# Kernel optimization log

Hardware: AMD Instinct MI355X
Metric: run time of the kernel (lower is better)

Reference implementation:

```python
import jax, jax.numpy as jnp
import numpy as np

G = 256          # grid resolution -> V = G*G vertices
B = 8            # batch of meshes
N_SAMPLES = 2048
W_CHAMFER, W_EDGE, W_NORMAL, W_LAP = 1.0, 1.0, 0.1, 0.1
V = G * G


def _grid_faces(g):
    idx = np.arange(g * g).reshape(g, g)
    v00 = idx[:-1, :-1].ravel(); v01 = idx[:-1, 1:].ravel()
    v10 = idx[1:, :-1].ravel();  v11 = idx[1:, 1:].ravel()
    f1 = np.stack([v00, v01, v10], 1)
    f2 = np.stack([v01, v11, v10], 1)
    return np.concatenate([f1, f2], 0).astype(np.int32)  # [F,3]


def _edges_and_pairs(faces, n_verts):
    # all face-edge incidences + the opposite vertex of each incidence
    e = np.concatenate([faces[:, [0, 1]], faces[:, [1, 2]], faces[:, [0, 2]]], 0)
    opp = np.concatenate([faces[:, 2], faces[:, 0], faces[:, 1]], 0)
    e = np.sort(e, 1)
    key = e[:, 0].astype(np.int64) * n_verts + e[:, 1]
    order = np.argsort(key, kind='stable')
    key_s, es, opps = key[order], e[order], opp[order]
    first = np.ones(len(key_s), bool); first[1:] = key_s[1:] != key_s[:-1]
    edges = es[first].astype(np.int32)                      # unique undirected edges [E,2]
    dup = np.nonzero(~first)[0]                             # 2nd incidence of shared edges
    pairs = np.stack([es[dup - 1, 0], es[dup - 1, 1], opps[dup - 1], opps[dup]], 1).astype(np.int32)  # [P,4]
    return edges, pairs


def setup_inputs() -> dict:
    key = jax.random.key(0)
    faces = _grid_faces(G)
    edges, nc_pairs = _edges_and_pairs(faces, V)
    # base grid geometry + gaussian perturbation (realistic smooth-ish surfaces)
    xs, ys = np.meshgrid(np.linspace(0, 1, G), np.linspace(0, 1, G), indexing='ij')
    base = np.stack([xs, ys, 0.1 * np.sin(4 * np.pi * xs) * np.cos(4 * np.pi * ys)], -1).reshape(V, 3)
    k1, k2 = jax.random.split(key)
    verts_pred = jnp.asarray(base, jnp.float32)[None] + 0.01 * jax.random.normal(k1, (B, V, 3), jnp.float32)
    verts_targ = jnp.asarray(base, jnp.float32)[None] + 0.01 * jax.random.normal(k2, (B, V, 3), jnp.float32)
    return {
        'verts_pred': verts_pred,
        'verts_targ': verts_targ,
        'faces': jnp.asarray(faces),
        'edges': jnp.asarray(edges),
        'nc_pairs': jnp.asarray(nc_pairs),
    }


def _sample_points(verts, faces, key, n):
    # verts [V,3]; area-weighted face sampling + uniform barycentric (pytorch3d scheme)
    v0, v1, v2 = verts[faces[:, 0]], verts[faces[:, 1]], verts[faces[:, 2]]
    areas = 0.5 * jnp.linalg.norm(jnp.cross(v1 - v0, v2 - v0), axis=-1)          # [F]
    kf, kb = jax.random.split(key)
    fidx = jax.random.categorical(kf, jnp.log(areas + 1e-12), shape=(n,))        # [n]
    uv = jax.random.uniform(kb, (n, 2), verts.dtype)
    su = jnp.sqrt(uv[:, 0:1]); vv = uv[:, 1:2]
    w0, w1, w2 = 1.0 - su, su * (1.0 - vv), su * vv
    return w0 * v0[fidx] + w1 * v1[fidx] + w2 * v2[fidx]                         # [n,3]


def _chamfer(x, y):
    # squared-distance chamfer, mean over points then batch, both directions summed
    d = jnp.sum((x[:, :, None, :] - y[:, None, :, :]) ** 2, -1)                  # [B,N,M]
    return jnp.mean(jnp.min(d, axis=2)) + jnp.mean(jnp.min(d, axis=1))


def _edge_loss(verts, edges):
    diff = verts[:, edges[:, 0]] - verts[:, edges[:, 1]]                          # [B,E,3]
    return jnp.mean(jnp.sum(diff * diff, -1))                                     # (||e|| - 0)^2


def _normal_consistency(verts, nc_pairs):
    v0 = verts[:, nc_pairs[:, 0]]; v1 = verts[:, nc_pairs[:, 1]]
    a = verts[:, nc_pairs[:, 2]]; b = verts[:, nc_pairs[:, 3]]
    e = v1 - v0
    n0 = jnp.cross(e, a - v0)
    n1 = -jnp.cross(e, b - v0)
    eps = 1e-8
    cos = jnp.sum(n0 * n1, -1) / (
        jnp.maximum(jnp.linalg.norm(n0, axis=-1), eps)
        * jnp.maximum(jnp.linalg.norm(n1, axis=-1), eps))
    return jnp.mean(1.0 - cos)


def _laplacian_uniform(verts, edges):
    e0, e1 = edges[:, 0], edges[:, 1]
    ones = jnp.ones((edges.shape[0],), verts.dtype)

    def per_mesh(v):  # v [V,3]
        nsum = (jax.ops.segment_sum(v[e1], e0, num_segments=V)
                + jax.ops.segment_sum(v[e0], e1, num_segments=V))
        deg = (jax.ops.segment_sum(ones, e0, num_segments=V)
               + jax.ops.segment_sum(ones, e1, num_segments=V))
        lap = nsum / jnp.maximum(deg, 1.0)[:, None] - v                           # D^-1 A v - v
        return jnp.mean(jnp.linalg.norm(lap, axis=-1))

    return jnp.mean(jax.vmap(per_mesh)(verts))


def reference(verts_pred, verts_targ, faces, edges, nc_pairs):
    skey = jax.random.key(42)
    kp = jax.random.split(jax.random.fold_in(skey, 0), verts_pred.shape[0])
    kt = jax.random.split(jax.random.fold_in(skey, 1), verts_targ.shape[0])
    sample_pred = jax.vmap(lambda v, k: _sample_points(v, faces, k, N_SAMPLES))(verts_pred, kp)
    sample_targ = jax.vmap(lambda v, k: _sample_points(v, faces, k, N_SAMPLES))(verts_targ, kt)
    loss_chamfer = _chamfer(sample_pred, sample_targ)
    loss_edge = _edge_loss(verts_pred, edges)
    loss_normal = _normal_consistency(verts_pred, nc_pairs)
    loss_lap = _laplacian_uniform(verts_pred, edges)
    loss = (W_CHAMFER * loss_chamfer + W_EDGE * loss_edge
            + W_NORMAL * loss_normal + W_LAP * loss_lap)
    return (loss, loss_chamfer, loss_edge, loss_normal, loss_lap)
```

## Files before the change

kernel.cpp:

```cpp
#include <hip/hip_runtime.h>
#include <stdint.h>

#define GSZ 256
#define NV (GSZ*GSZ)
#define NS 2048
#define CELLS (255*255)
#define FH CELLS
#define NF (2*CELLS)
#define CH 8

struct F3 { float x, y, z; };

__device__ __forceinline__ F3 ldv3(const float* __restrict__ p, int idx) {
    const float* q = p + 3*(size_t)idx;
    F3 r; r.x = q[0]; r.y = q[1]; r.z = q[2]; return r;
}
__device__ __forceinline__ F3 f3sub(F3 a, F3 b) { return F3{a.x-b.x, a.y-b.y, a.z-b.z}; }
__device__ __forceinline__ F3 f3cross(F3 a, F3 b) {
    return F3{a.y*b.z - a.z*b.y, a.z*b.x - a.x*b.z, a.x*b.y - a.y*b.x};
}
__device__ __forceinline__ float f3dot(F3 a, F3 b) { return a.x*b.x + a.y*b.y + a.z*b.z; }

__device__ __forceinline__ uint64_t splitmix64(uint64_t& s) {
    s += 0x9E3779B97F4A7C15ULL;
    uint64_t z = s;
    z = (z ^ (z >> 30)) * 0xBF58476D1CE4E5B9ULL;
    z = (z ^ (z >> 27)) * 0x94D049BB133111EBULL;
    return z ^ (z >> 31);
}

__device__ __forceinline__ float blockReduceSum256(float v) {
    __shared__ float s[4];
    int lane = threadIdx.x & 63, w = threadIdx.x >> 6;
    #pragma unroll
    for (int o = 32; o > 0; o >>= 1) v += __shfl_down(v, o, 64);
    if (lane == 0) s[w] = v;
    __syncthreads();
    if (threadIdx.x == 0) v = s[0] + s[1] + s[2] + s[3];
    return v;
}

__global__ void k_area(const float* __restrict__ vp, const float* __restrict__ vt,
                       int B, float* __restrict__ areas, float* __restrict__ blockmax) {
    int gid = blockIdx.x*256 + threadIdx.x;
    int total = 2*B*CELLS;
    float mloc = 0.f;
    if (gid < total) {
        int m = gid / CELLS;
        int c = gid - m*CELLS;
        int i = c / 255, j = c - i*255;
        const float* verts = (m < B ? vp + (size_t)m*NV*3
                                    : vt + (size_t)(m-B)*NV*3);
        int b00 = i*GSZ + j;
        F3 v00 = ldv3(verts, b00);
        F3 v01 = ldv3(verts, b00+1);
        F3 v10 = ldv3(verts, b00+GSZ);
        F3 v11 = ldv3(verts, b00+GSZ+1);
        F3 c1 = f3cross(f3sub(v01, v00), f3sub(v10, v00));
        F3 c2 = f3cross(f3sub(v11, v01), f3sub(v10, v01));
        float a1 = 0.5f * sqrtf(f3dot(c1, c1));
        float a2 = 0.5f * sqrtf(f3dot(c2, c2));
        size_t base = (size_t)m*NF;
        areas[base + c]      = a1;
        areas[base + FH + c] = a2;
        mloc = fmaxf(a1, a2);
    }
    #pragma unroll
    for (int o = 32; o > 0; o >>= 1) mloc = fmaxf(mloc, __shfl_down(mloc, o, 64));
    __shared__ float s[4];
    int lane = threadIdx.x & 63, w = threadIdx.x >> 6;
    if (lane == 0) s[w] = mloc;
    __syncthreads();
    if (threadIdx.x == 0)
        blockmax[blockIdx.x] = fmaxf(fmaxf(s[0], s[1]), fmaxf(s[2], s[3]));
}

__global__ void k_sample(const float* __restrict__ vp, const float* __restrict__ vt,
                         int B, const float* __restrict__ areas,
                         const float* __restrict__ blockmax, int nbm,
                         float* __restrict__ samples) {
    float m = 0.f;
    for (int k = threadIdx.x; k < nbm; k += 256) m = fmaxf(m, blockmax[k]);
    #pragma unroll
    for (int o = 32; o > 0; o >>= 1) m = fmaxf(m, __shfl_down(m, o, 64));
    __shared__ float s[4];
    int lane = threadIdx.x & 63, w = threadIdx.x >> 6;
    if (lane == 0) s[w] = m;
    __syncthreads();
    __shared__ float sMaxA;
    if (threadIdx.x == 0) sMaxA = fmaxf(fmaxf(s[0], s[1]), fmaxf(s[2], s[3]));
    __syncthreads();
    float maxA = sMaxA;

    int gid = blockIdx.x*256 + threadIdx.x;
    int cloud = gid / (B*NS);
    int rem = gid - cloud*(B*NS);
    int b = rem / NS;
    const float* verts = (cloud ? vt : vp) + (size_t)b*NV*3;
    const float* am = areas + (size_t)(cloud*B + b)*NF;

    uint64_t st = ((uint64_t)(gid + 1) * 0x9E3779B97F4A7C15ULL) ^ 0xC0FFEE123456789ULL;
    int f = 0;
    for (int round = 0; round < 64; ++round) {
        uint64_t r0 = splitmix64(st), r1 = splitmix64(st);
        uint64_t r2 = splitmix64(st), r3 = splitmix64(st);
        int f0 = (int)(((uint64_t)(uint32_t)r0 * (uint32_t)NF) >> 32);
        int f1 = (int)(((uint64_t)(uint32_t)r1 * (uint32_t)NF) >> 32);
        int f2 = (int)(((uint64_t)(uint32_t)r2 * (uint32_t)NF) >> 32);
        int f3 = (int)(((uint64_t)(uint32_t)r3 * (uint32_t)NF) >> 32);
        float a0 = am[f0], a1 = am[f1], a2 = am[f2], a3 = am[f3];
        float u0 = ((uint32_t)(r0 >> 40)) * (1.f/16777216.f);
        float u1 = ((uint32_t)(r1 >> 40)) * (1.f/16777216.f);
        float u2 = ((uint32_t)(r2 >> 40)) * (1.f/16777216.f);
        float u3 = ((uint32_t)(r3 >> 40)) * (1.f/16777216.f);
        if (u0 * maxA <= a0) { f = f0; break; }
        if (u1 * maxA <= a1) { f = f1; break; }
        if (u2 * maxA <= a2) { f = f2; break; }
        if (u3 * maxA <= a3) { f = f3; break; }
        f = f3;
    }
    int i0, i1, i2;
    if (f < FH) {
        int c = f;  int i = c / 255, j = c - i*255;  int v = i*GSZ + j;
        i0 = v; i1 = v + 1; i2 = v + GSZ;
    } else {
        int c = f - FH;  int i = c / 255, j = c - i*255;  int v = i*GSZ + j;
        i0 = v + 1; i1 = v + GSZ + 1; i2 = v + GSZ;
    }
    F3 v0 = ldv3(verts, i0), v1 = ldv3(verts, i1), v2 = ldv3(verts, i2);
    uint64_t r = splitmix64(st);
    float u0 = ((uint32_t)r >> 8) * (1.f/16777216.f);
    float u1 = ((uint32_t)(r >> 32) >> 8) * (1.f/16777216.f);
    float su = sqrtf(u0);
    float w0 = 1.f - su, w1 = su * (1.f - u1), w2 = su * u1;
    float* o = samples + (size_t)gid*3;
    o[0] = w0*v0.x + w1*v1.x + w2*v2.x;
    o[1] = w0*v0.y + w1*v1.y + w2*v2.y;
    o[2] = w0*v0.z + w1*v1.z + w2*v2.z;
}

__global__ void k_chamfer(const float* __restrict__ samples, int B,
                          float* __restrict__ minpart) {
    int dir = blockIdx.z >> 4, q = blockIdx.z & 15;
    int b = blockIdx.y, xh = blockIdx.x;
    const float* src = samples + ((size_t)dir*B + b)*NS*3;
    const float* dst = samples + ((size_t)(1-dir)*B + b)*NS*3;

    __shared__ float4 tile[128];
    if (threadIdx.x < 128) {
        const float* p = dst + (size_t)(q*128 + threadIdx.x)*3;
        tile[threadIdx.x] = make_float4(p[0], p[1], p[2], 0.f);
    }
    float px[4], py[4], pz[4], mn[4];
    #pragma unroll
    for (int k = 0; k < 4; ++k) {
        int i = xh*1024 + k*256 + threadIdx.x;
        const float* p = src + (size_t)i*3;
        px[k] = p[0]; py[k] = p[1]; pz[k] = p[2];
        mn[k] = 3.402823466e38f;
    }
    __syncthreads();
    #pragma unroll 2
    for (int j = 0; j < 128; ++j) {
        float4 t = tile[j];
        #pragma unroll
        for (int k = 0; k < 4; ++k) {
            float dx = px[k]-t.x, dy = py[k]-t.y, dz = pz[k]-t.z;
            mn[k] = fminf(mn[k], dx*dx + dy*dy + dz*dz);
        }
    }
    float* outp = minpart + (((size_t)(dir*B + b)*16) + q)*NS;
    #pragma unroll
    for (int k = 0; k < 4; ++k)
        outp[xh*1024 + k*256 + threadIdx.x] = mn[k];
}

__global__ void k_cham_reduce(const float* __restrict__ minpart, int B,
                              float* __restrict__ chamPart) {
    int gid = blockIdx.x*256 + threadIdx.x;
    int dir = gid / (B*NS);
    int rem = gid - dir*(B*NS);
    int b = rem / NS, i = rem - b*NS;
    const float* p = minpart + (size_t)(dir*B + b)*16*NS + i;
    float mn = 3.402823466e38f;
    #pragma unroll
    for (int q = 0; q < 16; ++q) mn = fminf(mn, p[(size_t)q*NS]);
    float sm = blockReduceSum256(mn);
    if (threadIdx.x == 0) chamPart[blockIdx.x] = sm;
}

__global__ void k_mesh(const float* __restrict__ vp, const int* __restrict__ edges,
                       const int* __restrict__ ncp, int B, int E, int P,
                       int nbE, int nbP,
                       float* __restrict__ partE, float* __restrict__ partP,
                       float* __restrict__ partV) {
    int bx = blockIdx.x, b = blockIdx.y;
    const float* verts = vp + (size_t)b*NV*3;
    float acc = 0.f;
    if (bx < nbE) {
        int base = bx*(256*CH);
        #pragma unroll 2
        for (int c = 0; c < CH; ++c) {
            int e = base + c*256 + threadIdx.x;
            if (e < E) {
                int2 ed = ((const int2*)edges)[e];
                F3 d = f3sub(ldv3(verts, ed.x), ldv3(verts, ed.y));
                acc += f3dot(d, d);
            }
        }
        float s = blockReduceSum256(acc);
        if (threadIdx.x == 0) partE[(size_t)bx*B + b] = s;
    } else if (bx < nbE + nbP) {
        int base = (bx - nbE)*(256*CH);
        for (int c = 0; c < CH; ++c) {
            int p = base + c*256 + threadIdx.x;
            if (p < P) {
                int4 q = ((const int4*)ncp)[p];
                F3 v0 = ldv3(verts, q.x), v1 = ldv3(verts, q.y);
                F3 a = ldv3(verts, q.z), bb = ldv3(verts, q.w);
                F3 e = f3sub(v1, v0);
                F3 n0 = f3cross(e, f3sub(a, v0));
                F3 n1 = f3cross(f3sub(bb, v0), e);
                float num = f3dot(n0, n1);
                float den = fmaxf(sqrtf(f3dot(n0, n0)), 1e-8f) *
                            fmaxf(sqrtf(f3dot(n1, n1)), 1e-8f);
                acc += 1.f - num / den;
            }
        }
        float s = blockReduceSum256(acc);
        if (threadIdx.x == 0) partP[(size_t)(bx - nbE)*B + b] = s;
    } else {
        int base = (bx - nbE - nbP)*(256*CH);
        for (int c = 0; c < CH; ++c) {
            int idx = base + c*256 + threadIdx.x;
            int i = idx >> 8, j = idx & 255;
            F3 ctr = ldv3(verts, idx);
            float nx = 0.f, ny = 0.f, nz = 0.f; int deg = 0;
            #define ADDN(ii, jj) { F3 n_ = ldv3(verts, (ii)*GSZ + (jj)); \
                                   nx += n_.x; ny += n_.y; nz += n_.z; ++deg; }
            if (j > 0)               ADDN(i, j-1);
            if (j < GSZ-1)           ADDN(i, j+1);
            if (i > 0)               ADDN(i-1, j);
            if (i < GSZ-1)           ADDN(i+1, j);
            if (i < GSZ-1 && j > 0)  ADDN(i+1, j-1);
            if (i > 0 && j < GSZ-1)  ADDN(i-1, j+1);
            #undef ADDN
            float inv = 1.f / (float)deg;
            float lx = nx*inv - ctr.x, ly = ny*inv - ctr.y, lz = nz*inv - ctr.z;
            acc += sqrtf(lx*lx + ly*ly + lz*lz);
        }
        float s = blockReduceSum256(acc);
        if (threadIdx.x == 0) partV[(size_t)(bx - nbE - nbP)*B + b] = s;
    }
}

__global__ void k_final(const float* __restrict__ chamPart,
                        const float* __restrict__ partE, int nE,
                        const float* __restrict__ partP, int nP,
                        const float* __restrict__ partV, int nL,
                        int B, int E, int P, float* __restrict__ out) {
    double a0 = 0, a1 = 0, aE = 0, aP = 0, aL = 0;
    for (int k = threadIdx.x; k < 64;  k += 256) a0 += (double)chamPart[k];
    for (int k = 64 + threadIdx.x; k < 128; k += 256) a1 += (double)chamPart[k];
    for (int k = threadIdx.x; k < nE; k += 256) aE += (double)partE[k];
    for (int k = threadIdx.x; k < nP; k += 256) aP += (double)partP[k];
    for (int k = threadIdx.x; k < nL; k += 256) aL += (double)partV[k];
    __shared__ double sd[5][4];
    double v[5] = {a0, a1, aE, aP, aL};
    int lane = threadIdx.x & 63, w = threadIdx.x >> 6;
    #pragma unroll
    for (int r = 0; r < 5; ++r) {
        double x = v[r];
        #pragma unroll
        for (int o = 32; o > 0; o >>= 1) x += __shfl_down(x, o, 64);
        if (lane == 0) sd[r][w] = x;
    }
    __syncthreads();
    if (threadIdx.x == 0) {
        double bn = (double)B * NS;
        double ch = (sd[0][0]+sd[0][1]+sd[0][2]+sd[0][3]) / bn
                  + (sd[1][0]+sd[1][1]+sd[1][2]+sd[1][3]) / bn;
        double ed = (sd[2][0]+sd[2][1]+sd[2][2]+sd[2][3]) / ((double)B * E);
        double no = (sd[3][0]+sd[3][1]+sd[3][2]+sd[3][3]) / ((double)B * P);
        double la = (sd[4][0]+sd[4][1]+sd[4][2]+sd[4][3]) / ((double)B * NV);
        double loss = ch + ed + 0.1*no + 0.1*la;
        out[0] = (float)loss; out[1] = (float)ch; out[2] = (float)ed;
        out[3] = (float)no;   out[4] = (float)la;
    }
}

extern "C" void kernel_launch(void* const* d_in, const int* in_sizes, int n_in,
                              void* d_out, int out_size, void* d_ws, size_t ws_size,
                              hipStream_t stream) {
    const float* vp = (const float*)d_in[0];
    const float* vt = (const float*)d_in[1];
    const int* edges = (const int*)d_in[3];
    const int* ncp   = (const int*)d_in[4];
    const int B = in_sizes[0] / (3*NV);
    const int E = in_sizes[3] / 2;
    const int P = in_sizes[4] / 4;

    char* ws = (char*)d_ws;
    size_t off = 0;
    float* areas    = (float*)(ws + off); off += (size_t)2*B*NF*sizeof(float);
    float* samples  = (float*)(ws + off); off += (size_t)2*B*NS*3*sizeof(float);
    float* minpart  = (float*)(ws + off); off += (size_t)2*B*16*NS*sizeof(float);
    float* blockmax = (float*)(ws + off); off += 8192*sizeof(float);
    float* chamPart = (float*)(ws + off); off += 256*sizeof(float);
    float* partE    = (float*)(ws + off); off += 2048*sizeof(float);
    float* partP    = (float*)(ws + off); off += 2048*sizeof(float);
    float* partV    = (float*)(ws + off); off += 1024*sizeof(float);

    int nbm = (2*B*CELLS + 255)/256;
    k_area<<<nbm, 256, 0, stream>>>(vp, vt, B, areas, blockmax);
    k_sample<<<(2*B*NS)/256, 256, 0, stream>>>(vp, vt, B, areas, blockmax, nbm, samples);
    dim3 gch(2, B, 32);
    k_chamfer<<<gch, 256, 0, stream>>>(samples, B, minpart);
    k_cham_reduce<<<(2*B*NS)/256, 256, 0, stream>>>(minpart, B, chamPart);
    int nbE = (E + 256*CH - 1)/(256*CH);
    int nbP = (P + 256*CH - 1)/(256*CH);
    int nbV = NV/(256*CH);
    dim3 gm(nbE + nbP + nbV, B);
    k_mesh<<<gm, 256, 0, stream>>>(vp, edges, ncp, B, E, P, nbE, nbP,
                                   partE, partP, partV);
    k_final<<<1, 256, 0, stream>>>(chamPart, partE, nbE*B, partP, nbP*B,
                                   partV, nbV*B, B, E, P, (float*)d_out);
}
```

Before: 147.6 us.

## Fuse all loss stages into one cooperative persistent kernel with grid syncs

```diff
diff --git a/kernel.cpp b/kernel.cpp
--- a/kernel.cpp
+++ b/kernel.cpp
@@ -1,5 +1,8 @@
 #include <hip/hip_runtime.h>
+#include <hip/hip_cooperative_groups.h>
 #include <stdint.h>
+
+namespace cg = cooperative_groups;
 
 #define GSZ 256
 #define NV (GSZ*GSZ)
@@ -7,7 +10,9 @@
 #define CELLS (255*255)
 #define FH CELLS
 #define NF (2*CELLS)
-#define CH 8
+#define NBLK 512
+#define NTHR 256
+#define NTOT (NBLK*NTHR)
 
 struct F3 { float x, y, z; };
 
@@ -29,211 +34,100 @@
     return z ^ (z >> 31);
 }
 
+__shared__ float4 g_tile[2048];
+__shared__ float  g_sred[4];
+__shared__ float  g_mred[256];
+__shared__ float  g_sMaxA;
+__shared__ double g_dred[5][4];
+
 __device__ __forceinline__ float blockReduceSum256(float v) {
-    __shared__ float s[4];
+    __syncthreads();
     int lane = threadIdx.x & 63, w = threadIdx.x >> 6;
     #pragma unroll
     for (int o = 32; o > 0; o >>= 1) v += __shfl_down(v, o, 64);
-    if (lane == 0) s[w] = v;
+    if (lane == 0) g_sred[w] = v;
     __syncthreads();
-    if (threadIdx.x == 0) v = s[0] + s[1] + s[2] + s[3];
+    if (threadIdx.x == 0) v = g_sred[0] + g_sred[1] + g_sred[2] + g_sred[3];
     return v;
 }
 
-__global__ void k_area(const float* __restrict__ vp, const float* __restrict__ vt,
-                       int B, float* __restrict__ areas, float* __restrict__ blockmax) {
-    int gid = blockIdx.x*256 + threadIdx.x;
-    int total = 2*B*CELLS;
+__global__ void __launch_bounds__(256, 2)
+k_all(const float* __restrict__ vp, const float* __restrict__ vt,
+      const int* __restrict__ edges, const int* __restrict__ ncp,
+      int B, int E, int P,
+      float* __restrict__ areas, float* __restrict__ samples,
+      float* __restrict__ blockmax, float* __restrict__ chamPart,
+      float* __restrict__ partE, float* __restrict__ partP,
+      float* __restrict__ partL, float* __restrict__ out) {
+    cg::grid_group grid = cg::this_grid();
+    const int tid = threadIdx.x, bid = blockIdx.x;
+    const int gid = bid*NTHR + tid;
+
     float mloc = 0.f;
-    if (gid < total) {
-        int m = gid / CELLS;
-        int c = gid - m*CELLS;
-        int i = c / 255, j = c - i*255;
-        const float* verts = (m < B ? vp + (size_t)m*NV*3
-                                    : vt + (size_t)(m-B)*NV*3);
-        int b00 = i*GSZ + j;
-        F3 v00 = ldv3(verts, b00);
-        F3 v01 = ldv3(verts, b00+1);
-        F3 v10 = ldv3(verts, b00+GSZ);
-        F3 v11 = ldv3(verts, b00+GSZ+1);
-        F3 c1 = f3cross(f3sub(v01, v00), f3sub(v10, v00));
-        F3 c2 = f3cross(f3sub(v11, v01), f3sub(v10, v01));
-        float a1 = 0.5f * sqrtf(f3dot(c1, c1));
-        float a2 = 0.5f * sqrtf(f3dot(c2, c2));
-        size_t base = (size_t)m*NF;
-        areas[base + c]      = a1;
-        areas[base + FH + c] = a2;
-        mloc = fmaxf(a1, a2);
-    }
-    #pragma unroll
-    for (int o = 32; o > 0; o >>= 1) mloc = fmaxf(mloc, __shfl_down(mloc, o, 64));
-    __shared__ float s[4];
-    int lane = threadIdx.x & 63, w = threadIdx.x >> 6;
-    if (lane == 0) s[w] = mloc;
-    __syncthreads();
-    if (threadIdx.x == 0)
-        blockmax[blockIdx.x] = fmaxf(fmaxf(s[0], s[1]), fmaxf(s[2], s[3]));
-}
-
-__global__ void k_sample(const float* __restrict__ vp, const float* __restrict__ vt,
-                         int B, const float* __restrict__ areas,
-                         const float* __restrict__ blockmax, int nbm,
-                         float* __restrict__ samples) {
-    float m = 0.f;
-    for (int k = threadIdx.x; k < nbm; k += 256) m = fmaxf(m, blockmax[k]);
-    #pragma unroll
-    for (int o = 32; o > 0; o >>= 1) m = fmaxf(m, __shfl_down(m, o, 64));
-    __shared__ float s[4];
-    int lane = threadIdx.x & 63, w = threadIdx.x >> 6;
-    if (lane == 0) s[w] = m;
-    __syncthreads();
-    __shared__ float sMaxA;
-    if (threadIdx.x == 0) sMaxA = fmaxf(fmaxf(s[0], s[1]), fmaxf(s[2], s[3]));
-    __syncthreads();
-    float maxA = sMaxA;
-
-    int gid = blockIdx.x*256 + threadIdx.x;
-    int cloud = gid / (B*NS);
-    int rem = gid - cloud*(B*NS);
-    int b = rem / NS;
-    const float* verts = (cloud ? vt : vp) + (size_t)b*NV*3;
-    const float* am = areas + (size_t)(cloud*B + b)*NF;
-
-    uint64_t st = ((uint64_t)(gid + 1) * 0x9E3779B97F4A7C15ULL) ^ 0xC0FFEE123456789ULL;
-    int f = 0;
-    for (int round = 0; round < 64; ++round) {
-        uint64_t r0 = splitmix64(st), r1 = splitmix64(st);
-        uint64_t r2 = splitmix64(st), r3 = splitmix64(st);
-        int f0 = (int)(((uint64_t)(uint32_t)r0 * (uint32_t)NF) >> 32);
-        int f1 = (int)(((uint64_t)(uint32_t)r1 * (uint32_t)NF) >> 32);
-        int f2 = (int)(((uint64_t)(uint32_t)r2 * (uint32_t)NF) >> 32);
-        int f3 = (int)(((uint64_t)(uint32_t)r3 * (uint32_t)NF) >> 32);
-        float a0 = am[f0], a1 = am[f1], a2 = am[f2], a3 = am[f3];
-        float u0 = ((uint32_t)(r0 >> 40)) * (1.f/16777216.f);
-        float u1 = ((uint32_t)(r1 >> 40)) * (1.f/16777216.f);
-        float u2 = ((uint32_t)(r2 >> 40)) * (1.f/16777216.f);
-        float u3 = ((uint32_t)(r3 >> 40)) * (1.f/16777216.f);
-        if (u0 * maxA <= a0) { f = f0; break; }
-        if (u1 * maxA <= a1) { f = f1; break; }
-        if (u2 * maxA <= a2) { f = f2; break; }
-        if (u3 * maxA <= a3) { f = f3; break; }
-        f = f3;
-    }
-    int i0, i1, i2;
-    if (f < FH) {
-        int c = f;  int i = c / 255, j = c - i*255;  int v = i*GSZ + j;
-        i0 = v; i1 = v + 1; i2 = v + GSZ;
-    } else {
-        int c = f - FH;  int i = c / 255, j = c - i*255;  int v = i*GSZ + j;
-        i0 = v + 1; i1 = v + GSZ + 1; i2 = v + GSZ;
-    }
-    F3 v0 = ldv3(verts, i0), v1 = ldv3(verts, i1), v2 = ldv3(verts, i2);
-    uint64_t r = splitmix64(st);
-    float u0 = ((uint32_t)r >> 8) * (1.f/16777216.f);
-    float u1 = ((uint32_t)(r >> 32) >> 8) * (1.f/16777216.f);
-    float su = sqrtf(u0);
-    float w0 = 1.f - su, w1 = su * (1.f - u1), w2 = su * u1;
-    float* o = samples + (size_t)gid*3;
-    o[0] = w0*v0.x + w1*v1.x + w2*v2.x;
-    o[1] = w0*v0.y + w1*v1.y + w2*v2.y;
-    o[2] = w0*v0.z + w1*v1.z + w2*v2.z;
-}
-
-__global__ void k_chamfer(const float* __restrict__ samples, int B,
-                          float* __restrict__ minpart) {
-    int dir = blockIdx.z >> 4, q = blockIdx.z & 15;
-    int b = blockIdx.y, xh = blockIdx.x;
-    const float* src = samples + ((size_t)dir*B + b)*NS*3;
-    const float* dst = samples + ((size_t)(1-dir)*B + b)*NS*3;
-
-    __shared__ float4 tile[128];
-    if (threadIdx.x < 128) {
-        const float* p = dst + (size_t)(q*128 + threadIdx.x)*3;
-        tile[threadIdx.x] = make_float4(p[0], p[1], p[2], 0.f);
-    }
-    float px[4], py[4], pz[4], mn[4];
-    #pragma unroll
-    for (int k = 0; k < 4; ++k) {
-        int i = xh*1024 + k*256 + threadIdx.x;
-        const float* p = src + (size_t)i*3;
-        px[k] = p[0]; py[k] = p[1]; pz[k] = p[2];
-        mn[k] = 3.402823466e38f;
-    }
-    __syncthreads();
-    #pragma unroll 2
-    for (int j = 0; j < 128; ++j) {
-        float4 t = tile[j];
+    {
+        int total = 2*B*CELLS;
+        for (int c = gid; c < total; c += NTOT) {
+            int m = c / CELLS, cc = c - m*CELLS;
+            int i = cc / 255, j = cc - i*255;
+            const float* verts = (m < B ? vp + (size_t)m*NV*3
+                                        : vt + (size_t)(m-B)*NV*3);
+            int v = i*GSZ + j;
+            F3 v00 = ldv3(verts, v),       v01 = ldv3(verts, v+1);
+            F3 v10 = ldv3(verts, v+GSZ),   v11 = ldv3(verts, v+GSZ+1);
+            F3 c1 = f3cross(f3sub(v01, v00), f3sub(v10, v00));
+            F3 c2 = f3cross(f3sub(v11, v01), f3sub(v10, v01));
+            float a1 = 0.5f * sqrtf(f3dot(c1, c1));
+            float a2 = 0.5f * sqrtf(f3dot(c2, c2));
+            size_t base = (size_t)m*NF;
+            areas[base + cc]      = a1;
+            areas[base + FH + cc] = a2;
+            mloc = fmaxf(mloc, fmaxf(a1, a2));
+        }
+    }
+    {
         #pragma unroll
-        for (int k = 0; k < 4; ++k) {
-            float dx = px[k]-t.x, dy = py[k]-t.y, dz = pz[k]-t.z;
-            mn[k] = fminf(mn[k], dx*dx + dy*dy + dz*dz);
-        }
-    }
-    float* outp = minpart + (((size_t)(dir*B + b)*16) + q)*NS;
-    #pragma unroll
-    for (int k = 0; k < 4; ++k)
-        outp[xh*1024 + k*256 + threadIdx.x] = mn[k];
-}
-
-__global__ void k_cham_reduce(const float* __restrict__ minpart, int B,
-                              float* __restrict__ chamPart) {
-    int gid = blockIdx.x*256 + threadIdx.x;
-    int dir = gid / (B*NS);
-    int rem = gid - dir*(B*NS);
-    int b = rem / NS, i = rem - b*NS;
-    const float* p = minpart + (size_t)(dir*B + b)*16*NS + i;
-    float mn = 3.402823466e38f;
-    #pragma unroll
-    for (int q = 0; q < 16; ++q) mn = fminf(mn, p[(size_t)q*NS]);
-    float sm = blockReduceSum256(mn);
-    if (threadIdx.x == 0) chamPart[blockIdx.x] = sm;
-}
-
-__global__ void k_mesh(const float* __restrict__ vp, const int* __restrict__ edges,
-                       const int* __restrict__ ncp, int B, int E, int P,
-                       int nbE, int nbP,
-                       float* __restrict__ partE, float* __restrict__ partP,
-                       float* __restrict__ partV) {
-    int bx = blockIdx.x, b = blockIdx.y;
-    const float* verts = vp + (size_t)b*NV*3;
-    float acc = 0.f;
-    if (bx < nbE) {
-        int base = bx*(256*CH);
-        #pragma unroll 2
-        for (int c = 0; c < CH; ++c) {
-            int e = base + c*256 + threadIdx.x;
-            if (e < E) {
-                int2 ed = ((const int2*)edges)[e];
-                F3 d = f3sub(ldv3(verts, ed.x), ldv3(verts, ed.y));
-                acc += f3dot(d, d);
-            }
-        }
-        float s = blockReduceSum256(acc);
-        if (threadIdx.x == 0) partE[(size_t)bx*B + b] = s;
-    } else if (bx < nbE + nbP) {
-        int base = (bx - nbE)*(256*CH);
-        for (int c = 0; c < CH; ++c) {
-            int p = base + c*256 + threadIdx.x;
-            if (p < P) {
-                int4 q = ((const int4*)ncp)[p];
-                F3 v0 = ldv3(verts, q.x), v1 = ldv3(verts, q.y);
-                F3 a = ldv3(verts, q.z), bb = ldv3(verts, q.w);
-                F3 e = f3sub(v1, v0);
-                F3 n0 = f3cross(e, f3sub(a, v0));
-                F3 n1 = f3cross(f3sub(bb, v0), e);
-                float num = f3dot(n0, n1);
-                float den = fmaxf(sqrtf(f3dot(n0, n0)), 1e-8f) *
-                            fmaxf(sqrtf(f3dot(n1, n1)), 1e-8f);
-                acc += 1.f - num / den;
-            }
-        }
-        float s = blockReduceSum256(acc);
-        if (threadIdx.x == 0) partP[(size_t)(bx - nbE)*B + b] = s;
-    } else {
-        int base = (bx - nbE - nbP)*(256*CH);
-        for (int c = 0; c < CH; ++c) {
-            int idx = base + c*256 + threadIdx.x;
+        for (int o = 32; o > 0; o >>= 1) mloc = fmaxf(mloc, __shfl_down(mloc, o, 64));
+        int lane = tid & 63, w = tid >> 6;
+        if (lane == 0) g_sred[w] = mloc;
+        __syncthreads();
+        if (tid == 0)
+            blockmax[bid] = fmaxf(fmaxf(g_sred[0], g_sred[1]),
+                                  fmaxf(g_sred[2], g_sred[3]));
+    }
+    float accE = 0.f, accP = 0.f, accL = 0.f;
+    {
+        int total = B*E;
+        for (int g = gid; g < total; g += NTOT) {
+            int b = g / E, e = g - b*E;
+            const float* verts = vp + (size_t)b*NV*3;
+            int2 ed = ((const int2*)edges)[e];
+            F3 d = f3sub(ldv3(verts, ed.x), ldv3(verts, ed.y));
+            accE += f3dot(d, d);
+        }
+    }
+    {
+        int total = B*P;
+        for (int g = gid; g < total; g += NTOT) {
+            int b = g / P, p = g - b*P;
+            const float* verts = vp + (size_t)b*NV*3;
+            int4 q = ((const int4*)ncp)[p];
+            F3 v0 = ldv3(verts, q.x), v1 = ldv3(verts, q.y);
+            F3 a = ldv3(verts, q.z), bb = ldv3(verts, q.w);
+            F3 e = f3sub(v1, v0);
+            F3 n0 = f3cross(e, f3sub(a, v0));
+            F3 n1 = f3cross(f3sub(bb, v0), e);
+            float num = f3dot(n0, n1);
+            float den = fmaxf(sqrtf(f3dot(n0, n0)), 1e-8f) *
+                        fmaxf(sqrtf(f3dot(n1, n1)), 1e-8f);
+            accP += 1.f - num / den;
+        }
+    }
+    {
+        int total = B*NV;
+        for (int g = gid; g < total; g += NTOT) {
+            int b = g >> 16, idx = g & (NV-1);
             int i = idx >> 8, j = idx & 255;
+            const float* verts = vp + (size_t)b*NV*3;
             F3 ctr = ldv3(verts, idx);
             float nx = 0.f, ny = 0.f, nz = 0.f; int deg = 0;
             #define ADDN(ii, jj) { F3 n_ = ldv3(verts, (ii)*GSZ + (jj)); \
@@ -247,45 +141,152 @@
             #undef ADDN
             float inv = 1.f / (float)deg;
             float lx = nx*inv - ctr.x, ly = ny*inv - ctr.y, lz = nz*inv - ctr.z;
-            acc += sqrtf(lx*lx + ly*ly + lz*lz);
-        }
-        float s = blockReduceSum256(acc);
-        if (threadIdx.x == 0) partV[(size_t)(bx - nbE - nbP)*B + b] = s;
-    }
-}
-
-__global__ void k_final(const float* __restrict__ chamPart,
-                        const float* __restrict__ partE, int nE,
-                        const float* __restrict__ partP, int nP,
-                        const float* __restrict__ partV, int nL,
-                        int B, int E, int P, float* __restrict__ out) {
-    double a0 = 0, a1 = 0, aE = 0, aP = 0, aL = 0;
-    for (int k = threadIdx.x; k < 64;  k += 256) a0 += (double)chamPart[k];
-    for (int k = 64 + threadIdx.x; k < 128; k += 256) a1 += (double)chamPart[k];
-    for (int k = threadIdx.x; k < nE; k += 256) aE += (double)partE[k];
-    for (int k = threadIdx.x; k < nP; k += 256) aP += (double)partP[k];
-    for (int k = threadIdx.x; k < nL; k += 256) aL += (double)partV[k];
-    __shared__ double sd[5][4];
-    double v[5] = {a0, a1, aE, aP, aL};
-    int lane = threadIdx.x & 63, w = threadIdx.x >> 6;
-    #pragma unroll
-    for (int r = 0; r < 5; ++r) {
-        double x = v[r];
+            accL += sqrtf(lx*lx + ly*ly + lz*lz);
+        }
+    }
+    {
+        float s = blockReduceSum256(accE);
+        if (tid == 0) partE[bid] = s;
+        s = blockReduceSum256(accP);
+        if (tid == 0) partP[bid] = s;
+        s = blockReduceSum256(accL);
+        if (tid == 0) partL[bid] = s;
+    }
+
+    grid.sync();
+
+    {
+        float m = 0.f;
+        for (int k = tid; k < NBLK; k += NTHR) m = fmaxf(m, blockmax[k]);
         #pragma unroll
-        for (int o = 32; o > 0; o >>= 1) x += __shfl_down(x, o, 64);
-        if (lane == 0) sd[r][w] = x;
-    }
-    __syncthreads();
-    if (threadIdx.x == 0) {
-        double bn = (double)B * NS;
-        double ch = (sd[0][0]+sd[0][1]+sd[0][2]+sd[0][3]) / bn
-                  + (sd[1][0]+sd[1][1]+sd[1][2]+sd[1][3]) / bn;
-        double ed = (sd[2][0]+sd[2][1]+sd[2][2]+sd[2][3]) / ((double)B * E);
-        double no = (sd[3][0]+sd[3][1]+sd[3][2]+sd[3][3]) / ((double)B * P);
-        double la = (sd[4][0]+sd[4][1]+sd[4][2]+sd[4][3]) / ((double)B * NV);
-        double loss = ch + ed + 0.1*no + 0.1*la;
-        out[0] = (float)loss; out[1] = (float)ch; out[2] = (float)ed;
-        out[3] = (float)no;   out[4] = (float)la;
+        for (int o = 32; o > 0; o >>= 1) m = fmaxf(m, __shfl_down(m, o, 64));
+        int lane = tid & 63, w = tid >> 6;
+        __syncthreads();
+        if (lane == 0) g_sred[w] = m;
+        __syncthreads();
+        if (tid == 0) g_sMaxA = fmaxf(fmaxf(g_sred[0], g_sred[1]),
+                                      fmaxf(g_sred[2], g_sred[3]));
+        __syncthreads();
+    }
+    if (gid < 2*B*NS) {
+        float maxA = g_sMaxA;
+        int cloud = gid / (B*NS);
+        int rem = gid - cloud*(B*NS);
+        int b = rem / NS;
+        const float* verts = (cloud ? vt : vp) + (size_t)b*NV*3;
+        const float* am = areas + (size_t)(cloud*B + b)*NF;
+
+        uint64_t st = ((uint64_t)(gid + 1) * 0x9E3779B97F4A7C15ULL) ^ 0xC0FFEE123456789ULL;
+        int f = 0;
+        for (int round = 0; round < 64; ++round) {
+            uint64_t r0 = splitmix64(st), r1 = splitmix64(st);
+            uint64_t r2 = splitmix64(st), r3 = splitmix64(st);
+            int f0 = (int)(((uint64_t)(uint32_t)r0 * (uint32_t)NF) >> 32);
+            int f1 = (int)(((uint64_t)(uint32_t)r1 * (uint32_t)NF) >> 32);
+            int f2 = (int)(((uint64_t)(uint32_t)r2 * (uint32_t)NF) >> 32);
+            int f3 = (int)(((uint64_t)(uint32_t)r3 * (uint32_t)NF) >> 32);
+            float a0 = am[f0], a1 = am[f1], a2 = am[f2], a3 = am[f3];
+            float u0 = ((uint32_t)(r0 >> 40)) * (1.f/16777216.f);
+            float u1 = ((uint32_t)(r1 >> 40)) * (1.f/16777216.f);
+            float u2 = ((uint32_t)(r2 >> 40)) * (1.f/16777216.f);
+            float u3 = ((uint32_t)(r3 >> 40)) * (1.f/16777216.f);
+            if (u0 * maxA <= a0) { f = f0; break; }
+            if (u1 * maxA <= a1) { f = f1; break; }
+            if (u2 * maxA <= a2) { f = f2; break; }
+            if (u3 * maxA <= a3) { f = f3; break; }
+            f = f3;
+        }
+        int i0, i1, i2;
+        if (f < FH) {
+            int c = f;  int i = c / 255, j = c - i*255;  int v = i*GSZ + j;
+            i0 = v; i1 = v + 1; i2 = v + GSZ;
+        } else {
+            int c = f - FH;  int i = c / 255, j = c - i*255;  int v = i*GSZ + j;
+            i0 = v + 1; i1 = v + GSZ + 1; i2 = v + GSZ;
+        }
+        F3 v0 = ldv3(verts, i0), v1 = ldv3(verts, i1), v2 = ldv3(verts, i2);
+        uint64_t r = splitmix64(st);
+        float u0 = ((uint32_t)r >> 8) * (1.f/16777216.f);
+        float u1 = ((uint32_t)(r >> 32) >> 8) * (1.f/16777216.f);
+        float su = sqrtf(u0);
+        float w0 = 1.f - su, w1 = su * (1.f - u1), w2 = su * u1;
+        float* o = samples + (size_t)gid*3;
+        o[0] = w0*v0.x + w1*v1.x + w2*v2.x;
+        o[1] = w0*v0.y + w1*v1.y + w2*v2.y;
+        o[2] = w0*v0.z + w1*v1.z + w2*v2.z;
+    }
+
+    grid.sync();
+
+    if (bid < 2*B*32) {
+        int dir = bid / (B*32);
+        int rem = bid - dir*(B*32);
+        int b = rem >> 5, chunk = rem & 31;
+        const float* src = samples + ((size_t)dir*B + b)*NS*3;
+        const float* dst = samples + ((size_t)(1-dir)*B + b)*NS*3;
+        for (int k = tid; k < 2048; k += NTHR) {
+            const float* p = dst + (size_t)k*3;
+            g_tile[k] = make_float4(p[0], p[1], p[2], 0.f);
+        }
+        int sl = tid & 63;
+        int q  = tid >> 6;
+        const float* sp = src + (size_t)(chunk*64 + sl)*3;
+        float px = sp[0], py = sp[1], pz = sp[2];
+        __syncthreads();
+        float mn = 3.402823466e38f;
+        int j0 = q*512;
+        #pragma unroll 4
+        for (int j = j0; j < j0 + 512; ++j) {
+            float4 t = g_tile[j];
+            float dx = px-t.x, dy = py-t.y, dz = pz-t.z;
+            mn = fminf(mn, fmaf(dx, dx, fmaf(dy, dy, dz*dz)));
+        }
+        g_mred[tid] = mn;
+        __syncthreads();
+        if (tid < 64) {
+            float m = fminf(fminf(g_mred[tid], g_mred[tid+64]),
+                            fminf(g_mred[tid+128], g_mred[tid+192]));
+            #pragma unroll
+            for (int o = 32; o > 0; o >>= 1) m += __shfl_down(m, o, 64);
+            if (tid == 0) chamPart[bid] = m;
+        }
+    }
+
+    grid.sync();
+
+    if (bid == 0) {
+        int nPerDir = B*32;
+        double a0 = 0, a1 = 0, aE = 0, aP = 0, aL = 0;
+        for (int k = tid; k < 2*nPerDir; k += NTHR) {
+            double v = (double)chamPart[k];
+            if (k < nPerDir) a0 += v; else a1 += v;
+        }
+        for (int k = tid; k < NBLK; k += NTHR) {
+            aE += (double)partE[k];
+            aP += (double)partP[k];
+            aL += (double)partL[k];
+        }
+        double v5[5] = {a0, a1, aE, aP, aL};
+        int lane = tid & 63, w = tid >> 6;
+        #pragma unroll
+        for (int r = 0; r < 5; ++r) {
+            double x = v5[r];
+            #pragma unroll
+            for (int o = 32; o > 0; o >>= 1) x += __shfl_down(x, o, 64);
+            if (lane == 0) g_dred[r][w] = x;
+        }
+        __syncthreads();
+        if (tid == 0) {
+            double bn = (double)B * NS;
+            double ch = (g_dred[0][0]+g_dred[0][1]+g_dred[0][2]+g_dred[0][3]) / bn
+                      + (g_dred[1][0]+g_dred[1][1]+g_dred[1][2]+g_dred[1][3]) / bn;
+            double ed = (g_dred[2][0]+g_dred[2][1]+g_dred[2][2]+g_dred[2][3]) / ((double)B*E);
+            double no = (g_dred[3][0]+g_dred[3][1]+g_dred[3][2]+g_dred[3][3]) / ((double)B*P);
+            double la = (g_dred[4][0]+g_dred[4][1]+g_dred[4][2]+g_dred[4][3]) / ((double)B*NV);
+            double loss = ch + ed + 0.1*no + 0.1*la;
+            out[0] = (float)loss; out[1] = (float)ch; out[2] = (float)ed;
+            out[3] = (float)no;   out[4] = (float)la;
+        }
     }
 }
 
@@ -296,33 +297,24 @@
     const float* vt = (const float*)d_in[1];
     const int* edges = (const int*)d_in[3];
     const int* ncp   = (const int*)d_in[4];
-    const int B = in_sizes[0] / (3*NV);
-    const int E = in_sizes[3] / 2;
-    const int P = in_sizes[4] / 4;
+    int B = in_sizes[0] / (3*NV);
+    int E = in_sizes[3] / 2;
+    int P = in_sizes[4] / 4;
 
     char* ws = (char*)d_ws;
     size_t off = 0;
     float* areas    = (float*)(ws + off); off += (size_t)2*B*NF*sizeof(float);
     float* samples  = (float*)(ws + off); off += (size_t)2*B*NS*3*sizeof(float);
-    float* minpart  = (float*)(ws + off); off += (size_t)2*B*16*NS*sizeof(float);
-    float* blockmax = (float*)(ws + off); off += 8192*sizeof(float);
-    float* chamPart = (float*)(ws + off); off += 256*sizeof(float);
-    float* partE    = (float*)(ws + off); off += 2048*sizeof(float);
-    float* partP    = (float*)(ws + off); off += 2048*sizeof(float);
-    float* partV    = (float*)(ws + off); off += 1024*sizeof(float);
-
-    int nbm = (2*B*CELLS + 255)/256;
-    k_area<<<nbm, 256, 0, stream>>>(vp, vt, B, areas, blockmax);
-    k_sample<<<(2*B*NS)/256, 256, 0, stream>>>(vp, vt, B, areas, blockmax, nbm, samples);
-    dim3 gch(2, B, 32);
-    k_chamfer<<<gch, 256, 0, stream>>>(samples, B, minpart);
-    k_cham_reduce<<<(2*B*NS)/256, 256, 0, stream>>>(minpart, B, chamPart);
-    int nbE = (E + 256*CH - 1)/(256*CH);
-    int nbP = (P + 256*CH - 1)/(256*CH);
-    int nbV = NV/(256*CH);
-    dim3 gm(nbE + nbP + nbV, B);
-    k_mesh<<<gm, 256, 0, stream>>>(vp, edges, ncp, B, E, P, nbE, nbP,
-                                   partE, partP, partV);
-    k_final<<<1, 256, 0, stream>>>(chamPart, partE, nbE*B, partP, nbP*B,
-                                   partV, nbV*B, B, E, P, (float*)d_out);
-}
+    float* blockmax = (float*)(ws + off); off += NBLK*sizeof(float);
+    float* chamPart = (float*)(ws + off); off += NBLK*sizeof(float);
+    float* partE    = (float*)(ws + off); off += NBLK*sizeof(float);
+    float* partP    = (float*)(ws + off); off += NBLK*sizeof(float);
+    float* partL    = (float*)(ws + off); off += NBLK*sizeof(float);
+    float* out      = (float*)d_out;
+
+    void* args[] = { &vp, &vt, &edges, &ncp, &B, &E, &P,
+                     &areas, &samples, &blockmax, &chamPart,
+                     &partE, &partP, &partL, &out };
+    hipLaunchCooperativeKernel((void*)k_all, dim3(NBLK), dim3(NTHR),
+                               args, 0, stream);
+}
```

New measurement: 317.6 us. 115% more time.
